# Kernel optimization log

Hardware: AMD Instinct MI355X
Metric: run time of the kernel (lower is better)

Reference implementation:

```python
import jax, jax.numpy as jnp
import numpy as np

NUM_NODES = 2048
NUM_FEATURES = 512
NUM_CLASSES = 128
INF = 1e9  # finite stand-in for float('inf'): identical shortest-path results on
           # connected positive-weight graphs, but keeps gradients NaN-free


def bellman_ford(adj_matrix, source_node):
    """Min-plus Bellman-Ford relaxation.

    Returns:
      distances:    (N, N) where distances[v, i] = shortest dist source->v using <= i edges
      predecessors: (N,)   argmin predecessor on the final relaxation
      has_negative_cycle: () bool, True if an N-th relaxation still improves
    """
    n = adj_matrix.shape[0]
    init = jnp.full((n,), INF, dtype=adj_matrix.dtype).at[source_node].set(0.0)

    def step(dist, _):
        # new[v] = min(dist[v], min_u dist[u] + w(u, v))  -- one relaxation sweep
        new = jnp.minimum(dist, jnp.min(dist[:, None] + adj_matrix, axis=0))
        return new, new

    step = jax.checkpoint(step)  # O(N) saved state per step instead of O(N^2)
    final, hist = jax.lax.scan(step, init, None, length=n - 1)

    distances = jnp.concatenate([init[:, None], hist.T], axis=1)  # (N, N)

    relax = jnp.min(final[:, None] + adj_matrix, axis=0)
    predecessors = jnp.where(relax <= final,
                             jnp.argmin(final[:, None] + adj_matrix, axis=0),
                             -1)
    has_negative_cycle = jnp.any(jnp.minimum(final, relax) < final)
    return distances, predecessors, has_negative_cycle


def setup_inputs() -> dict:
    key = jax.random.key(0)
    k1, k2, k3 = jax.random.split(key, 3)
    adj_matrix = jax.random.uniform(k1, (NUM_NODES, NUM_NODES), dtype=jnp.float32)
    node_embedding = jax.random.normal(k2, (NUM_NODES, NUM_FEATURES), dtype=jnp.float32)
    fc_weight = jax.random.normal(k3, (NUM_CLASSES, NUM_FEATURES + NUM_NODES), dtype=jnp.float32) * 0.02
    fc_bias = jnp.zeros((NUM_CLASSES,), dtype=jnp.float32)
    return {
        "adj_matrix": adj_matrix,
        "node_embedding": node_embedding,
        "fc_weight": fc_weight,
        "fc_bias": fc_bias,
        "source_node": 0,
    }


def reference(adj_matrix, node_embedding, fc_weight, fc_bias, source_node):
    distances, predecessors, has_negative_cycle = bellman_ford(adj_matrix, source_node)
    # node_embedding plays the role of Embedding(arange(N)) lookup = full table
    node_features = jnp.concatenate([node_embedding, distances], axis=1)  # (N, F+N)
    output = node_features @ fc_weight.T + fc_bias  # (N, C)
    return output, has_negative_cycle
```

## Files before the change

### kernel.cpp

```cpp
#include <hip/hip_runtime.h>
#include <hip/hip_cooperative_groups.h>

namespace cg = cooperative_groups;

#define NN   2048
#define FF   512
#define CC   128
#define WROW 2560
#define INFV 1.0e9f
#define NB   128
#define NT   1024
#define BN   16

#define AL64(p)   __hip_atomic_load((p),  __ATOMIC_RELAXED, __HIP_MEMORY_SCOPE_AGENT)
#define AS64(p,v) __hip_atomic_store((p), (v), __ATOMIC_RELAXED, __HIP_MEMORY_SCOPE_AGENT)

struct WS {
    unsigned long long D[2][NN];
    unsigned long long Suf[CC];
};

__device__ __forceinline__ unsigned long long pk(unsigned tag, float v) {
    return ((unsigned long long)tag << 32) | (unsigned long long)__float_as_uint(v);
}
__device__ __forceinline__ unsigned tg(unsigned long long e) { return (unsigned)(e >> 32); }
__device__ __forceinline__ float    vl(unsigned long long e) { return __uint_as_float((unsigned)e); }

__global__ __launch_bounds__(NT, 1)
void bf_tagged(const float* __restrict__ adj,
               const float* __restrict__ emb,
               const float* __restrict__ W,
               const float* __restrict__ bias,
               const int*   __restrict__ srcp,
               float*       __restrict__ out,
               WS* ws, int out_size)
{
    __shared__ __align__(16) float adjT[BN * NN];
    __shared__ __align__(16) float dist[NN];
    __shared__ float wcol[2][CC];
    __shared__ float red[BN];
    __shared__ float dprevP[2][BN];
    __shared__ unsigned redc[BN];

    const int tid = threadIdx.x;
    const int b   = blockIdx.x;
    const int src = *srcp;
    const int q  = (b & 7) * 16 + (b >> 3);
    const int vb = q * BN;

    if (tid < BN) {
        int v = vb + tid;
        AS64(&ws->D[0][v], pk(0u, (v == src) ? 0.0f : INFV));
        AS64(&ws->D[1][v], pk(0xFFFFFFFFu, 0.0f));
        if (tid == 0) AS64(&ws->Suf[b], 0ull);
    }

    #pragma unroll
    for (int it = 0; it < (NN * 4) / NT; ++it) {
        int r = tid + NT * it;
        int u = r >> 2, qc = (r & 3) * 4;
        float4 a = *(const float4*)(adj + (size_t)u * NN + vb + qc);
        adjT[(qc + 0) * NN + u] = a.x;
        adjT[(qc + 1) * NN + u] = a.y;
        adjT[(qc + 2) * NN + u] = a.z;
        adjT[(qc + 3) * NN + u] = a.w;
    }
    dist[tid]      = (tid == src) ? 0.0f : INFV;
    dist[tid + NT] = ((tid + NT) == src) ? 0.0f : INFV;
    if (tid < BN) {
        float d = ((vb + tid) == src) ? 0.0f : INFV;
        dprevP[0][tid] = d; dprevP[1][tid] = d;
    }

    const int vown = tid >> 6;
    const int lane = tid & 63;
    const int c0 = 2 * lane, c1 = c0 + 1;
    const int vE = vb + (tid & 15);
    const int cE = (2 * (tid >> 4)) & 127;
    const int u2 = 2 * tid;
    float ea0 = 0.0f, ea1 = 0.0f;

    float acc0, acc1;
    { float d0 = ((vb + vown) == src) ? 0.0f : INFV;
      acc0 = d0 * W[(size_t)c0 * WROW + FF];
      acc1 = d0 * W[(size_t)c1 * WROW + FF]; }

    cg::this_grid().sync();

    int kconv = -1, hneg = 0;

    for (int s = 1; s <= NN; ++s) {
        unsigned long long* Dq = ws->D[(s - 1) & 1];
        const unsigned want = (unsigned)(s - 1);
        if (vown == 1 && s < NN) {
            wcol[s & 1][lane]      = W[(size_t)lane * WROW + FF + s];
            wcol[s & 1][64 + lane] = W[(size_t)(64 + lane) * WROW + FF + s];
        }
        unsigned long long e0 = AL64(&Dq[u2]), e1 = AL64(&Dq[u2 + 1]);
        while (tg(e0) != want) { __builtin_amdgcn_s_sleep(1); e0 = AL64(&Dq[u2]); }
        while (tg(e1) != want) { __builtin_amdgcn_s_sleep(1); e1 = AL64(&Dq[u2 + 1]); }
        float n0 = vl(e0), n1 = vl(e1);
        unsigned ch = (n0 != dist[u2]) | (n1 != dist[u2 + 1]);
        dist[u2] = n0; dist[u2 + 1] = n1;
        unsigned long long bal = __ballot(ch != 0);
        if (lane == 0) redc[vown] = (bal != 0ull) ? 1u : 0u;
        __syncthreads();

        unsigned any = 0;
        #pragma unroll
        for (int w = 0; w < BN; ++w) any |= redc[w];
        if (s >= 2 && !any) { kconv = s - 1; break; }

        float m = 4.0e9f;
        const float* ar = adjT + vown * NN;
        #pragma unroll
        for (int k = 0; k < 8; ++k) {
            int u = 4 * lane + 256 * k;
            float4 dd = *(const float4*)(dist + u);
            float4 aa = *(const float4*)(ar + u);
            m = fminf(m, fminf(fminf(dd.x + aa.x, dd.y + aa.y),
                               fminf(dd.z + aa.z, dd.w + aa.w)));
        }
        #pragma unroll
        for (int st = 1; st < 64; st <<= 1) m = fminf(m, __shfl_xor(m, st, 64));
        if (lane == 0) red[vown] = m;
        __syncthreads();

        float nv = fminf(dprevP[(s - 1) & 1][vown], red[vown]);
        if (tid < BN) {
            float nv2 = fminf(dprevP[(s - 1) & 1][tid], red[tid]);
            AS64(&ws->D[s & 1][vb + tid], pk((unsigned)s, nv2));
            dprevP[s & 1][tid] = nv2;
        }
        if (s < NN) {
            acc0 = fmaf(nv, wcol[s & 1][c0], acc0);
            acc1 = fmaf(nv, wcol[s & 1][c1], acc1);
        }
        if (s - 1 < 16) {
            int i0 = 32 * (s - 1);
            const float4* ep = (const float4*)(emb + (size_t)vE * FF + i0);
            const float4* wa = (const float4*)(W + (size_t)cE * WROW + i0);
            const float4* wb = (const float4*)(W + (size_t)(cE + 1) * WROW + i0);
            #pragma unroll
            for (int j = 0; j < 8; ++j) {
                float4 e = ep[j], x = wa[j], y = wb[j];
                ea0 += e.x*x.x + e.y*x.y + e.z*x.z + e.w*x.w;
                ea1 += e.x*y.x + e.y*y.y + e.z*y.z + e.w*y.w;
            }
        }
    }

    if (kconv < 0) {
        unsigned long long* Dq = ws->D[NN & 1];
        unsigned long long e0 = AL64(&Dq[u2]), e1 = AL64(&Dq[u2 + 1]);
        while (tg(e0) != NN) { __builtin_amdgcn_s_sleep(1); e0 = AL64(&Dq[u2]); }
        while (tg(e1) != NN) { __builtin_amdgcn_s_sleep(1); e1 = AL64(&Dq[u2 + 1]); }
        unsigned ch = (vl(e0) != dist[u2]) | (vl(e1) != dist[u2 + 1]);
        unsigned long long bal = __ballot(ch != 0);
        if (lane == 0) redc[vown] = (bal != 0ull) ? 1u : 0u;
        __syncthreads();
        unsigned any = 0;
        #pragma unroll
        for (int w = 0; w < BN; ++w) any |= redc[w];
        hneg = any ? 1 : 0;
    } else if (kconv >= 1 && kconv <= NN - 2) {
        float ssum = 0.0f;
        for (int i = kconv + 1 + tid; i <= NN - 1; i += NT)
            ssum += W[(size_t)b * WROW + FF + i];
        #pragma unroll
        for (int st = 1; st < 64; st <<= 1) ssum += __shfl_xor(ssum, st, 64);
        if (lane == 0) red[vown] = ssum;
        __syncthreads();
        if (tid == 0) {
            float x = 0.0f;
            #pragma unroll
            for (int w = 0; w < BN; ++w) x += red[w];
            AS64(&ws->Suf[b], pk(0x40000000u + (unsigned)kconv, x));
        }
        const unsigned wantS = 0x40000000u + (unsigned)kconv;
        unsigned long long s0 = AL64(&ws->Suf[c0]), s1 = AL64(&ws->Suf[c1]);
        while (tg(s0) != wantS) { __builtin_amdgcn_s_sleep(1); s0 = AL64(&ws->Suf[c0]); }
        while (tg(s1) != wantS) { __builtin_amdgcn_s_sleep(1); s1 = AL64(&ws->Suf[c1]); }
        float dv = dist[vb + vown];
        acc0 = fmaf(dv, vl(s0), acc0);
        acc1 = fmaf(dv, vl(s1), acc1);
    }

    for (int chk = (kconv < 0 ? 16 : (kconv < 16 ? kconv : 16)); chk < 16; ++chk) {
        int i0 = 32 * chk;
        const float4* ep = (const float4*)(emb + (size_t)vE * FF + i0);
        const float4* wa = (const float4*)(W + (size_t)cE * WROW + i0);
        const float4* wb = (const float4*)(W + (size_t)(cE + 1) * WROW + i0);
        #pragma unroll
        for (int j = 0; j < 8; ++j) {
            float4 e = ep[j], x = wa[j], y = wb[j];
            ea0 += e.x*x.x + e.y*x.y + e.z*x.z + e.w*x.w;
            ea1 += e.x*y.x + e.y*y.y + e.z*y.z + e.w*y.w;
        }
    }

    __syncthreads();
    float* comb = adjT;
    comb[(tid & 15) * 129 + cE]     = ea0;
    comb[(tid & 15) * 129 + cE + 1] = ea1;
    __syncthreads();
    float o0 = acc0 + comb[vown * 129 + c0] + bias[c0];
    float o1 = acc1 + comb[vown * 129 + c1] + bias[c1];
    *(float2*)(out + (size_t)(vb + vown) * CC + c0) = make_float2(o0, o1);
    if (b == 0 && tid == 0 && out_size > NN * CC)
        out[NN * CC] = hneg ? 1.0f : 0.0f;
}

extern "C" void kernel_launch(void* const* d_in, const int* in_sizes, int n_in,
                              void* d_out, int out_size, void* d_ws, size_t ws_size,
                              hipStream_t stream) {
    const float* adj  = (const float*)d_in[0];
    const float* emb  = (const float*)d_in[1];
    const float* W    = (const float*)d_in[2];
    const float* bias = (const float*)d_in[3];
    const int*   srcp = (const int*)d_in[4];
    float* outp = (float*)d_out;
    WS* ws = (WS*)d_ws;
    int osz = out_size;

    void* args[] = { (void*)&adj, (void*)&emb, (void*)&W, (void*)&bias,
                     (void*)&srcp, (void*)&outp, (void*)&ws, (void*)&osz };
    hipLaunchCooperativeKernel((const void*)bf_tagged,
                               dim3(NB), dim3(NT), args, 0, stream);
}
```

Baseline: 161.6 us.

## Replace per-element tagged polling with per-block flag handshake and drop grid sync

Drops the cooperative launch and the grid-wide sync. Each step's distances are now published as raw 32-bit values, and a single per-block step counter is written after a vmcnt wait and a block barrier. Consumers poll 128 block flags, one per thread, instead of spinning on 2048 tagged 64-bit entries, and then read the packed distance pairs with one 64-bit load. The change also moves the embedding partial products before the min-plus reduction, keeps the previous distance in a register, and pads the flags and suffix slots. The risks are relying on all blocks being co-resident without a cooperative launch, the correctness of the memory ordering (relaxed stores plus s_waitcnt), and possible stale flags across calls, which the MAGIC initialisation is meant to guard against.

```diff
diff --git a/kernel.cpp b/kernel.cpp
--- a/kernel.cpp
+++ b/kernel.cpp
@@ -1,7 +1,4 @@
 #include <hip/hip_runtime.h>
-#include <hip/hip_cooperative_groups.h>
-
-namespace cg = cooperative_groups;
 
 #define NN   2048
 #define FF   512
@@ -11,13 +8,17 @@
 #define NB   128
 #define NT   1024
 #define BN   16
-
+#define MAGIC 0xB00F5EEDu
+
+#define AL32(p)   __hip_atomic_load((p),  __ATOMIC_RELAXED, __HIP_MEMORY_SCOPE_AGENT)
+#define AS32(p,v) __hip_atomic_store((p), (v), __ATOMIC_RELAXED, __HIP_MEMORY_SCOPE_AGENT)
 #define AL64(p)   __hip_atomic_load((p),  __ATOMIC_RELAXED, __HIP_MEMORY_SCOPE_AGENT)
 #define AS64(p,v) __hip_atomic_store((p), (v), __ATOMIC_RELAXED, __HIP_MEMORY_SCOPE_AGENT)
 
 struct WS {
-    unsigned long long D[2][NN];
-    unsigned long long Suf[CC];
+    unsigned long long D64[2][NN / 2];
+    unsigned T[2][NB][16];
+    unsigned long long Suf[CC][8];
 };
 
 __device__ __forceinline__ unsigned long long pk(unsigned tag, float v) {
@@ -27,7 +28,7 @@
 __device__ __forceinline__ float    vl(unsigned long long e) { return __uint_as_float((unsigned)e); }
 
 __global__ __launch_bounds__(NT, 1)
-void bf_tagged(const float* __restrict__ adj,
+void bf_nosync(const float* __restrict__ adj,
                const float* __restrict__ emb,
                const float* __restrict__ W,
                const float* __restrict__ bias,
@@ -37,26 +38,25 @@
 {
     __shared__ __align__(16) float adjT[BN * NN];
     __shared__ __align__(16) float dist[NN];
-    __shared__ float wcol[2][CC];
-    __shared__ float red[BN];
-    __shared__ float dprevP[2][BN];
-    __shared__ unsigned redc[BN];
+    __shared__ float    wcol[CC];
+    __shared__ float    red16[16];
+    __shared__ unsigned redc[16];
 
     const int tid = threadIdx.x;
     const int b   = blockIdx.x;
     const int src = *srcp;
-    const int q  = (b & 7) * 16 + (b >> 3);
-    const int vb = q * BN;
-
-    if (tid < BN) {
-        int v = vb + tid;
-        AS64(&ws->D[0][v], pk(0u, (v == src) ? 0.0f : INFV));
-        AS64(&ws->D[1][v], pk(0xFFFFFFFFu, 0.0f));
-        if (tid == 0) AS64(&ws->Suf[b], 0ull);
-    }
+    const int q   = (b & 7) * 16 + (b >> 3);
+    const int vb  = q * BN;
+
+    if (tid == 0) AS32(&ws->T[1][b][0], MAGIC);
+    if (tid < BN)
+        AS32(((unsigned*)&ws->D64[0][0]) + (vb + tid),
+             __float_as_uint(((vb + tid) == src) ? 0.0f : INFV));
+    if (tid < 64) asm volatile("s_waitcnt vmcnt(0)" ::: "memory");
+    if (tid == 0) AS32(&ws->T[0][b][0], MAGIC);
 
     #pragma unroll
-    for (int it = 0; it < (NN * 4) / NT; ++it) {
+    for (int it = 0; it < 8; ++it) {
         int r = tid + NT * it;
         int u = r >> 2, qc = (r & 3) * 4;
         float4 a = *(const float4*)(adj + (size_t)u * NN + vb + qc);
@@ -67,75 +67,50 @@
     }
     dist[tid]      = (tid == src) ? 0.0f : INFV;
     dist[tid + NT] = ((tid + NT) == src) ? 0.0f : INFV;
-    if (tid < BN) {
-        float d = ((vb + tid) == src) ? 0.0f : INFV;
-        dprevP[0][tid] = d; dprevP[1][tid] = d;
-    }
+    __syncthreads();
 
     const int vown = tid >> 6;
     const int lane = tid & 63;
     const int c0 = 2 * lane, c1 = c0 + 1;
     const int vE = vb + (tid & 15);
     const int cE = (2 * (tid >> 4)) & 127;
-    const int u2 = 2 * tid;
     float ea0 = 0.0f, ea1 = 0.0f;
+    float dprev_r = ((vb + vown) == src) ? 0.0f : INFV;
 
     float acc0, acc1;
-    { float d0 = ((vb + vown) == src) ? 0.0f : INFV;
+    { float d0 = dprev_r;
       acc0 = d0 * W[(size_t)c0 * WROW + FF];
       acc1 = d0 * W[(size_t)c1 * WROW + FF]; }
 
-    cg::this_grid().sync();
-
     int kconv = -1, hneg = 0;
 
     for (int s = 1; s <= NN; ++s) {
-        unsigned long long* Dq = ws->D[(s - 1) & 1];
-        const unsigned want = (unsigned)(s - 1);
-        if (vown == 1 && s < NN) {
-            wcol[s & 1][lane]      = W[(size_t)lane * WROW + FF + s];
-            wcol[s & 1][64 + lane] = W[(size_t)(64 + lane) * WROW + FF + s];
-        }
-        unsigned long long e0 = AL64(&Dq[u2]), e1 = AL64(&Dq[u2 + 1]);
-        while (tg(e0) != want) { __builtin_amdgcn_s_sleep(1); e0 = AL64(&Dq[u2]); }
-        while (tg(e1) != want) { __builtin_amdgcn_s_sleep(1); e1 = AL64(&Dq[u2 + 1]); }
-        float n0 = vl(e0), n1 = vl(e1);
-        unsigned ch = (n0 != dist[u2]) | (n1 != dist[u2 + 1]);
-        dist[u2] = n0; dist[u2 + 1] = n1;
-        unsigned long long bal = __ballot(ch != 0);
-        if (lane == 0) redc[vown] = (bal != 0ull) ? 1u : 0u;
-        __syncthreads();
-
+        const int p = (s - 1) & 1;
+        if (tid < NB) {
+            const unsigned want = (s == 1) ? MAGIC : (unsigned)(s - 1);
+            unsigned f = AL32(&ws->T[p][tid][0]);
+            while (f != want) { __builtin_amdgcn_s_sleep(1); f = AL32(&ws->T[p][tid][0]); }
+        }
+        __syncthreads();
+        if (s < NN && vown == 1) {
+            wcol[lane]      = W[(size_t)lane * WROW + FF + s];
+            wcol[64 + lane] = W[(size_t)(64 + lane) * WROW + FF + s];
+        }
+        {
+            unsigned long long e = AL64(&ws->D64[p][tid]);
+            float n0 = __uint_as_float((unsigned)e);
+            float n1 = __uint_as_float((unsigned)(e >> 32));
+            unsigned ch = (n0 != dist[2 * tid]) | (n1 != dist[2 * tid + 1]);
+            dist[2 * tid] = n0; dist[2 * tid + 1] = n1;
+            unsigned long long bal = __ballot(ch != 0);
+            if (lane == 0) redc[vown] = (bal != 0ull) ? 1u : 0u;
+        }
+        __syncthreads();
         unsigned any = 0;
         #pragma unroll
-        for (int w = 0; w < BN; ++w) any |= redc[w];
+        for (int w = 0; w < 16; ++w) any |= redc[w];
         if (s >= 2 && !any) { kconv = s - 1; break; }
 
-        float m = 4.0e9f;
-        const float* ar = adjT + vown * NN;
-        #pragma unroll
-        for (int k = 0; k < 8; ++k) {
-            int u = 4 * lane + 256 * k;
-            float4 dd = *(const float4*)(dist + u);
-            float4 aa = *(const float4*)(ar + u);
-            m = fminf(m, fminf(fminf(dd.x + aa.x, dd.y + aa.y),
-                               fminf(dd.z + aa.z, dd.w + aa.w)));
-        }
-        #pragma unroll
-        for (int st = 1; st < 64; st <<= 1) m = fminf(m, __shfl_xor(m, st, 64));
-        if (lane == 0) red[vown] = m;
-        __syncthreads();
-
-        float nv = fminf(dprevP[(s - 1) & 1][vown], red[vown]);
-        if (tid < BN) {
-            float nv2 = fminf(dprevP[(s - 1) & 1][tid], red[tid]);
-            AS64(&ws->D[s & 1][vb + tid], pk((unsigned)s, nv2));
-            dprevP[s & 1][tid] = nv2;
-        }
-        if (s < NN) {
-            acc0 = fmaf(nv, wcol[s & 1][c0], acc0);
-            acc1 = fmaf(nv, wcol[s & 1][c1], acc1);
-        }
         if (s - 1 < 16) {
             int i0 = 32 * (s - 1);
             const float4* ep = (const float4*)(emb + (size_t)vE * FF + i0);
@@ -148,20 +123,49 @@
                 ea1 += e.x*y.x + e.y*y.y + e.z*y.z + e.w*y.w;
             }
         }
+
+        float m = 4.0e9f;
+        const float* ar = adjT + vown * NN;
+        #pragma unroll
+        for (int k = 0; k < 8; ++k) {
+            int u = 4 * lane + 256 * k;
+            float4 dd = *(const float4*)(dist + u);
+            float4 aa = *(const float4*)(ar + u);
+            m = fminf(m, fminf(fminf(dd.x + aa.x, dd.y + aa.y),
+                               fminf(dd.z + aa.z, dd.w + aa.w)));
+        }
+        #pragma unroll
+        for (int st = 1; st < 64; st <<= 1) m = fminf(m, __shfl_xor(m, st, 64));
+        float nv = fminf(dprev_r, m);
+        dprev_r = nv;
+
+        if (lane == 0)
+            AS32(((unsigned*)&ws->D64[s & 1][0]) + (vb + vown), __float_as_uint(nv));
+        asm volatile("s_waitcnt vmcnt(0)" ::: "memory");
+        __syncthreads();
+        if (tid == 0) AS32(&ws->T[s & 1][b][0], (unsigned)s);
+
+        if (s < NN) {
+            acc0 = fmaf(nv, wcol[c0], acc0);
+            acc1 = fmaf(nv, wcol[c1], acc1);
+        }
     }
 
     if (kconv < 0) {
-        unsigned long long* Dq = ws->D[NN & 1];
-        unsigned long long e0 = AL64(&Dq[u2]), e1 = AL64(&Dq[u2 + 1]);
-        while (tg(e0) != NN) { __builtin_amdgcn_s_sleep(1); e0 = AL64(&Dq[u2]); }
-        while (tg(e1) != NN) { __builtin_amdgcn_s_sleep(1); e1 = AL64(&Dq[u2 + 1]); }
-        unsigned ch = (vl(e0) != dist[u2]) | (vl(e1) != dist[u2 + 1]);
+        if (tid < NB) {
+            unsigned f = AL32(&ws->T[0][tid][0]);
+            while (f != (unsigned)NN) { __builtin_amdgcn_s_sleep(1); f = AL32(&ws->T[0][tid][0]); }
+        }
+        __syncthreads();
+        unsigned long long e = AL64(&ws->D64[0][tid]);
+        unsigned ch = (__uint_as_float((unsigned)e) != dist[2 * tid]) |
+                      (__uint_as_float((unsigned)(e >> 32)) != dist[2 * tid + 1]);
         unsigned long long bal = __ballot(ch != 0);
         if (lane == 0) redc[vown] = (bal != 0ull) ? 1u : 0u;
         __syncthreads();
         unsigned any = 0;
         #pragma unroll
-        for (int w = 0; w < BN; ++w) any |= redc[w];
+        for (int w = 0; w < 16; ++w) any |= redc[w];
         hneg = any ? 1 : 0;
     } else if (kconv >= 1 && kconv <= NN - 2) {
         float ssum = 0.0f;
@@ -169,18 +173,19 @@
             ssum += W[(size_t)b * WROW + FF + i];
         #pragma unroll
         for (int st = 1; st < 64; st <<= 1) ssum += __shfl_xor(ssum, st, 64);
-        if (lane == 0) red[vown] = ssum;
+        if (lane == 0) red16[vown] = ssum;
         __syncthreads();
         if (tid == 0) {
             float x = 0.0f;
             #pragma unroll
-            for (int w = 0; w < BN; ++w) x += red[w];
-            AS64(&ws->Suf[b], pk(0x40000000u + (unsigned)kconv, x));
+            for (int w = 0; w < 16; ++w) x += red16[w];
+            AS64(&ws->Suf[b][0], pk(0x40000000u + (unsigned)kconv, x));
         }
         const unsigned wantS = 0x40000000u + (unsigned)kconv;
-        unsigned long long s0 = AL64(&ws->Suf[c0]), s1 = AL64(&ws->Suf[c1]);
-        while (tg(s0) != wantS) { __builtin_amdgcn_s_sleep(1); s0 = AL64(&ws->Suf[c0]); }
-        while (tg(s1) != wantS) { __builtin_amdgcn_s_sleep(1); s1 = AL64(&ws->Suf[c1]); }
+        unsigned long long s0 = AL64(&ws->Suf[c0][0]);
+        while (tg(s0) != wantS) { __builtin_amdgcn_s_sleep(1); s0 = AL64(&ws->Suf[c0][0]); }
+        unsigned long long s1 = AL64(&ws->Suf[c1][0]);
+        while (tg(s1) != wantS) { __builtin_amdgcn_s_sleep(1); s1 = AL64(&ws->Suf[c1][0]); }
         float dv = dist[vb + vown];
         acc0 = fmaf(dv, vl(s0), acc0);
         acc1 = fmaf(dv, vl(s1), acc1);
@@ -223,8 +228,6 @@
     WS* ws = (WS*)d_ws;
     int osz = out_size;
 
-    void* args[] = { (void*)&adj, (void*)&emb, (void*)&W, (void*)&bias,
-                     (void*)&srcp, (void*)&outp, (void*)&ws, (void*)&osz };
-    hipLaunchCooperativeKernel((const void*)bf_tagged,
-                               dim3(NB), dim3(NT), args, 0, stream);
+    bf_nosync<<<dim3(NB), dim3(NT), 0, stream>>>(adj, emb, W, bias, srcp,
+                                                 outp, ws, osz);
 }
```

Result: faster. 142.9 us (-11.6%).
